# Kernel tuning notes

Hardware: AMD Instinct MI355X
Metric: run time of the kernel (lower is better)

## Reference

```python
import jax, jax.numpy as jnp
import numpy as np

DELAY = 4
SKIP = 2
NF = 8
HS = 256
EPS = 1e-5


def setup_inputs() -> dict:
    key = jax.random.key(0)
    ks = jax.random.split(key, 11)
    B, NP, NO, T = 16, 512, 512, 2048
    predictor = jax.random.normal(ks[0], (B, NP, T), dtype=jnp.float32)
    to_order = jax.random.normal(ks[1], (B, NO, T), dtype=jnp.float32)
    trilinear = jax.random.normal(ks[2], (NF, NO, NP), dtype=jnp.float32) / np.float32(np.sqrt(NP * NO))
    w_o = jax.random.normal(ks[3], (HS, NO), dtype=jnp.float32) / np.float32(np.sqrt(NO))
    b_o = jax.random.normal(ks[4], (HS,), dtype=jnp.float32) * 0.01
    w_p = jax.random.normal(ks[5], (HS, NP), dtype=jnp.float32) / np.float32(np.sqrt(NP))
    b_p = jax.random.normal(ks[6], (HS,), dtype=jnp.float32) * 0.01
    bn_gamma = jnp.ones((HS,), dtype=jnp.float32)
    bn_beta = jnp.zeros((HS,), dtype=jnp.float32)
    w_out = jax.random.normal(ks[7], (NF, HS), dtype=jnp.float32) / np.float32(np.sqrt(HS))
    b_out = jax.random.normal(ks[8], (NF,), dtype=jnp.float32) * 0.01
    return {"predictor": predictor, "to_order": to_order, "trilinear": trilinear,
            "w_o": w_o, "b_o": b_o, "w_p": w_p, "b_p": b_p,
            "bn_gamma": bn_gamma, "bn_beta": bn_beta, "w_out": w_out, "b_out": b_out}


def reference(predictor, to_order, trilinear, w_o, b_o, w_p, b_p, bn_gamma, bn_beta, w_out, b_out):
    B, NP, T = predictor.shape
    NO = to_order.shape[1]
    tot_latency = DELAY + SKIP * (NF - 1)
    T_r = T - tot_latency
    pred = predictor[:, :, :T_r]          # (B, np, Tr)
    too = to_order[:, :, DELAY:]          # (B, no, T - delay)
    # predictor_product[b,k,t,m] = sum_p pred[b,p,t] * trilinear[k,m,p]
    pp = jnp.einsum('bpt,kmp->bktm', pred, trilinear)           # (B, nf, Tr, no)
    win = jnp.stack([too[:, :, j * SKIP: j * SKIP + T_r] for j in range(NF)], axis=1)  # (B, nf, no, Tr)
    inner = jnp.einsum('bjmt,bktm->bjkt', win, pp)              # (B, nf, nf, Tr)
    # conv1d (kernel 1) heads
    o_proj = jnp.einsum('hm,bmt->bht', w_o, too) + b_o[None, :, None]    # (B, hs, T - delay)
    p_proj = jnp.einsum('hp,bpt->bht', w_p, pred) + b_p[None, :, None]   # (B, hs, Tr)
    o_win = jnp.stack([o_proj[:, :, j * SKIP: j * SKIP + T_r] for j in range(NF)], axis=1)  # (B, nf, hs, Tr)
    h = jax.nn.relu(o_win + p_proj[:, None])                    # (B, nf, hs, Tr)
    # BatchNorm1d (training-mode batch stats) over (B*nf, hs, Tr): stats over axes (0,1,3)
    mean = h.mean(axis=(0, 1, 3), keepdims=True)
    var = h.var(axis=(0, 1, 3), keepdims=True)
    h = (h - mean) * jax.lax.rsqrt(var + EPS) * bn_gamma[None, None, :, None] + bn_beta[None, None, :, None]
    head = jnp.einsum('kh,bjht->bjkt', w_out, h) + b_out[None, None, :, None]
    inner = inner + head
    log_probs = jax.nn.log_softmax(inner, axis=2)               # (B, nf, nf, Tr)
    correct = jnp.einsum('bjjt->bjt', log_probs)                # diagonal j == k
    return correct.mean(axis=2).mean(axis=0)                    # (nf,)
```

## Files before the change

### kernel.cpp

```cpp
#include <hip/hip_runtime.h>
#include <math.h>

constexpr int B_  = 16;
constexpr int NP_ = 512;
constexpr int NO_ = 512;
constexpr int T_  = 2048;
constexpr int NF_ = 8;
constexpr int HS_ = 256;
constexpr int TR_ = 2030;
constexpr int TO_ = 2044;
constexpr int OPLD_ = 2048;
constexpr float EPS_ = 1e-5f;

typedef short bf16x8 __attribute__((ext_vector_type(8)));
typedef float f32x16 __attribute__((ext_vector_type(16)));

__device__ __forceinline__ unsigned short f2bf(float f) {
  union { float f; unsigned int u; } v; v.f = f;
  unsigned int r = v.u + 0x7fffu + ((v.u >> 16) & 1u);
  return (unsigned short)(r >> 16);
}
__device__ __forceinline__ float bf2f(unsigned short u) {
  union { unsigned int u; float f; } v; v.u = ((unsigned int)u) << 16;
  return v.f;
}

typedef const __attribute__((address_space(1))) unsigned int* gas_u32;
typedef __attribute__((address_space(3))) unsigned int* las_u32;
__device__ __forceinline__ void gl16(const void* g, void* l) {
  __builtin_amdgcn_global_load_lds((gas_u32)g, (las_u32)l, 16, 0, 0);
}


__global__ __launch_bounds__(256) void transpose_cvt(
    const float* __restrict__ in, unsigned short* __restrict__ outb) {
  __shared__ float tile[64][65];
  const int c0 = blockIdx.x * 64;
  const int r0 = blockIdx.y * 64;
  const int b  = blockIdx.z;
  const float* ib = in + (size_t)b * 512 * 2048;
  unsigned short* ob = outb + (size_t)b * 2048 * 512;
  for (int i = threadIdx.x; i < 64 * 16; i += 256) {
    const int r = i >> 4, c4 = (i & 15) * 4;
    float4 v = *(const float4*)(ib + (size_t)(r0 + r) * 2048 + c0 + c4);
    tile[r][c4 + 0] = v.x; tile[r][c4 + 1] = v.y;
    tile[r][c4 + 2] = v.z; tile[r][c4 + 3] = v.w;
  }
  __syncthreads();
  for (int i = threadIdx.x; i < 64 * 8; i += 256) {
    const int c = i >> 3, r8 = (i & 7) * 8;
    unsigned int pk[4];
    #pragma unroll
    for (int e = 0; e < 4; ++e)
      pk[e] = (unsigned int)f2bf(tile[r8 + 2 * e][c]) |
              ((unsigned int)f2bf(tile[r8 + 2 * e + 1][c]) << 16);
    *(uint4*)(ob + (size_t)(c0 + c) * 512 + r0 + r8) = *(uint4*)pk;
  }
}

__global__ __launch_bounds__(256) void cvt_bf16(
    const float* __restrict__ in, unsigned short* __restrict__ out, int n) {
  const int i = (blockIdx.x * 256 + threadIdx.x) * 4;
  if (i < n) {
    float4 v = *(const float4*)(in + i);
    ushort4 o; o.x = f2bf(v.x); o.y = f2bf(v.y); o.z = f2bf(v.z); o.w = f2bf(v.w);
    *(ushort4*)(out + i) = o;
  }
}

__global__ __launch_bounds__(256, 2) void proj_mfma(
    const unsigned short* __restrict__ Wbf,
    const unsigned short* __restrict__ Xt,
    const float* __restrict__ bias,
    unsigned short* __restrict__ out,
    int Tlen, int toff) {
  __shared__ char smem[65536];
  char* const Ab[2] = { smem, smem + 16384 };
  char* const Bb[2] = { smem + 32768, smem + 49152 };
  const int tid = threadIdx.x;
  const int l = tid & 63, wv = tid >> 6;
  const int h = l >> 5, tl = l & 31;
  const int mq = wv >> 1, tq = wv & 1;
  const int t0 = blockIdx.x * 128;
  const int m0 = blockIdx.y * 128;
  const int b  = blockIdx.z;
  const unsigned short* Xb = Xt + (size_t)b * T_ * 512;

  int aSrc[4], bSrc[4], ldsO[4];
  #pragma unroll
  for (int i = 0; i < 4; ++i) {
    const int q = (wv << 8) + (i << 6) + l;
    const int r = q >> 3, c8s = (q & 7) ^ (r & 7);
    aSrc[i] = (m0 + r) * 512 + (c8s << 3);
    const int row = min(t0 + toff + r, T_ - 1);
    bSrc[i] = row * 512 + (c8s << 3);
    ldsO[i] = ((wv << 8) + (i << 6)) << 4;
  }

  f32x16 acc[2][2];
  #pragma unroll
  for (int i = 0; i < 2; ++i)
    #pragma unroll
    for (int jj = 0; jj < 2; ++jj)
      #pragma unroll
      for (int e = 0; e < 16; ++e) acc[i][jj][e] = 0.f;

  #pragma unroll
  for (int i = 0; i < 4; ++i) gl16(Wbf + aSrc[i], Ab[0] + ldsO[i]);
  #pragma unroll
  for (int i = 0; i < 4; ++i) gl16(Xb + bSrc[i], Bb[0] + ldsO[i]);
  asm volatile("s_waitcnt vmcnt(0)" ::: "memory");
  __builtin_amdgcn_s_barrier();

  #pragma unroll
  for (int ps = 0; ps < 8; ++ps) {
    const int cb = ps & 1;
    if (ps < 7) {
      const int p0 = (ps + 1) << 6;
      #pragma unroll
      for (int i = 0; i < 4; ++i) gl16(Wbf + p0 + aSrc[i], Ab[cb ^ 1] + ldsO[i]);
      #pragma unroll
      for (int i = 0; i < 4; ++i) gl16(Xb + p0 + bSrc[i], Bb[cb ^ 1] + ldsO[i]);
    }
    const unsigned short* As = (const unsigned short*)Ab[cb];
    const unsigned short* Bs = (const unsigned short*)Bb[cb];
    #pragma unroll
    for (int s = 0; s < 4; ++s) {
      const int k8 = 2 * s + h;
      bf16x8 af[2], bfr[2];
      #pragma unroll
      for (int mt = 0; mt < 2; ++mt) {
        const int rm = 64 * mq + 32 * mt + tl;
        af[mt] = *(const bf16x8*)(As + rm * 64 + ((k8 ^ (rm & 7)) << 3));
      }
      #pragma unroll
      for (int nt = 0; nt < 2; ++nt) {
        const int rt = 64 * tq + 32 * nt + tl;
        bfr[nt] = *(const bf16x8*)(Bs + rt * 64 + ((k8 ^ (rt & 7)) << 3));
      }
      #pragma unroll
      for (int mt = 0; mt < 2; ++mt)
        #pragma unroll
        for (int nt = 0; nt < 2; ++nt)
          acc[mt][nt] = __builtin_amdgcn_mfma_f32_32x32x16_bf16(
              af[mt], bfr[nt], acc[mt][nt], 0, 0, 0);
    }
    asm volatile("s_waitcnt vmcnt(0)" ::: "memory");
    __builtin_amdgcn_s_barrier();
  }
  #pragma unroll
  for (int mt = 0; mt < 2; ++mt)
    #pragma unroll
    for (int nt = 0; nt < 2; ++nt)
      #pragma unroll
      for (int r = 0; r < 16; ++r) {
        const int hs = m0 + 64 * mq + 32 * mt + (r & 3) + 8 * (r >> 2) + 4 * h;
        const int t  = t0 + 64 * tq + 32 * nt + tl;
        if (t < Tlen)
          out[((size_t)b * HS_ + hs) * OPLD_ + t] = f2bf(acc[mt][nt][r] + bias[hs]);
      }
}

__global__ __launch_bounds__(256, 2) void inner_mfma(
    const unsigned short* __restrict__ pred_t,
    const unsigned short* __restrict__ too_t,
    const unsigned short* __restrict__ tri_bf,
    float* __restrict__ inner) {
  __shared__ char smem[77824];
  char* const Pb[2] = { smem, smem + 16384 };
  char* const Tb[2] = { smem + 32768, smem + 49152 };
  char* const TOOM  = smem + 65536;
  char* const TAIL  = smem + 32768;
  const int tid = threadIdx.x;
  const int l = tid & 63, wv = tid >> 6;
  const int h = l >> 5, tl = l & 31;
  const int t0 = blockIdx.x * 128;
  const int kf0 = blockIdx.y * 2;
  const int b  = blockIdx.z;
  const unsigned short* predB = pred_t + (size_t)b * T_ * NP_;
  const unsigned short* tooB  = too_t  + (size_t)b * T_ * NO_;
  const unsigned short* triK  = tri_bf + (size_t)kf0 * NO_ * NP_;

  int pSrc[4], pLds[4];
  #pragma unroll
  for (int i = 0; i < 4; ++i) {
    const int q = (wv << 8) + (i << 6) + l;
    const int r = q >> 3, c8s = (q & 7) ^ (r & 7);
    pSrc[i] = (t0 + r) * NP_ + (c8s << 3);
    pLds[i] = ((wv << 8) + (i << 6)) << 4;
  }
  int tSrc[4], tLds[4];
  #pragma unroll
  for (int i = 0; i < 4; ++i) {
    const int q = (wv << 8) + (i << 6) + l;
    const int f = q >> 9, qq = q & 511;
    const int r = qq >> 3, c8s = (qq & 7) ^ (r & 7);
    tSrc[i] = f * (NO_ * NP_) + r * NP_ + (c8s << 3);
    tLds[i] = ((wv << 8) + (i << 6)) << 4;
  }
  int oSrc[3], oLds[3];
  #pragma unroll
  for (int i = 0; i < 3; ++i) {
    const int q = wv * 192 + (i << 6) + l;
    const int r = q >> 3, c8s = (q & 7) ^ (r & 7);
    oSrc[i] = (t0 + r) * NO_ + (c8s << 3);
    oLds[i] = (wv * 192 + (i << 6)) << 4;
  }
  int aSrcT[4], aLdsT[4];
  {
    const int ws = (wv >= 2) ? (wv - 2) : 0;
    #pragma unroll
    for (int i = 0; i < 4; ++i) {
      const int q = (ws << 8) + (i << 6) + l;
      const int r = 96 + (q >> 3), c8s = (q & 7) ^ (r & 7);
      aSrcT[i] = min(t0 + r, T_ - 1) * NO_ + (c8s << 3);
      aLdsT[i] = ((ws << 8) + (i << 6)) << 4;
    }
  }

  f32x16 Sacc[2][2];
  #pragma unroll
  for (int f = 0; f < 2; ++f)
    #pragma unroll
    for (int ct = 0; ct < 2; ++ct)
      #pragma unroll
      for (int e = 0; e < 16; ++e) Sacc[f][ct][e] = 0.f;

  for (int mc = 0; mc < 8; ++mc) {
    const int m0 = mc << 6;
    const int mOff = m0 * NP_;
    __builtin_amdgcn_s_barrier();
    #pragma unroll
    for (int i = 0; i < 3; ++i) gl16(tooB + m0 + oSrc[i], TOOM + oLds[i]);
    #pragma unroll
    for (int i = 0; i < 4; ++i) gl16(triK + mOff + tSrc[i], Tb[0] + tLds[i]);
    #pragma unroll
    for (int i = 0; i < 4; ++i) gl16(predB + pSrc[i], Pb[0] + pLds[i]);
    asm volatile("s_waitcnt vmcnt(0)" ::: "memory");
    __builtin_amdgcn_s_barrier();

    f32x16 Qacc[2][2];
    #pragma unroll
    for (int f = 0; f < 2; ++f)
      #pragma unroll
      for (int mt = 0; mt < 2; ++mt)
        #pragma unroll
        for (int e = 0; e < 16; ++e) Qacc[f][mt][e] = 0.f;

    #pragma unroll
    for (int ps = 0; ps < 8; ++ps) {
      const int cb = ps & 1;
      if (ps < 7) {
        const int p1 = (ps + 1) << 6;
        #pragma unroll
        for (int i = 0; i < 4; ++i)
          gl16(triK + mOff + p1 + tSrc[i], Tb[cb ^ 1] + tLds[i]);
        #pragma unroll
        for (int i = 0; i < 4; ++i)
          gl16(predB + p1 + pSrc[i], Pb[cb ^ 1] + pLds[i]);
      }
      const unsigned short* predS = (const unsigned short*)Pb[cb];
      const unsigned short* triS  = (const unsigned short*)Tb[cb];
      #pragma unroll
      for (int s = 0; s < 4; ++s) {
        const int k8 = 2 * s + h;
        const int rb = (wv << 5) + tl;
        const bf16x8 bp = *(const bf16x8*)(predS + rb * 64 + ((k8 ^ (rb & 7)) << 3));
        #pragma unroll
        for (int mt = 0; mt < 2; ++mt) {
          const int rm = (mt << 5) + tl;
          const int co = rm * 64 + ((k8 ^ (rm & 7)) << 3);
          const bf16x8 a0 = *(const bf16x8*)(triS + co);
          const bf16x8 a1 = *(const bf16x8*)(triS + 2048 + co);
          Qacc[0][mt] = __builtin_amdgcn_mfma_f32_32x32x16_bf16(a0, bp, Qacc[0][mt], 0, 0, 0);
          Qacc[1][mt] = __builtin_amdgcn_mfma_f32_32x32x16_bf16(a1, bp, Qacc[1][mt], 0, 0, 0);
        }
      }
      if (ps == 7 && wv >= 2) {
        #pragma unroll
        for (int i = 0; i < 4; ++i)
          gl16(tooB + m0 + aSrcT[i], TAIL + aLdsT[i]);
      }
      asm volatile("s_waitcnt vmcnt(0)" ::: "memory");
      __builtin_amdgcn_s_barrier();
    }
    #pragma unroll
    for (int f = 0; f < 2; ++f) {
      unsigned short* QSw = (unsigned short*)(Pb[f] + (wv << 12));
      #pragma unroll
      for (int mt = 0; mt < 2; ++mt)
        #pragma unroll
        for (int rp = 0; rp < 8; ++rp) {
          const int r = rp << 1;
          const int m = (mt << 5) + (r & 3) + ((r >> 2) << 3) + (h << 2);
          const int c8 = m >> 3, ml = m & 7;
          const int rX = (tl & 24) | ((tl ^ c8) & 7);
          const unsigned int pk = (unsigned int)f2bf(Qacc[f][mt][r]) |
                                  ((unsigned int)f2bf(Qacc[f][mt][r + 1]) << 16);
          *(unsigned int*)(QSw + (((c8 << 5) + rX) << 3) + ml) = pk;
        }
    }
    #pragma unroll
    for (int s = 0; s < 4; ++s) {
      const int k8 = 2 * s + h;
      bf16x8 atoo[2];
      #pragma unroll
      for (int ct = 0; ct < 2; ++ct) {
        const int rbase = (wv + ct) << 5;
        const int rr = rbase + tl;
        const unsigned short* tb = (rbase < 96)
            ? (const unsigned short*)TOOM + (size_t)rr * 64
            : (const unsigned short*)TAIL + (size_t)(rr - 96) * 64;
        atoo[ct] = *(const bf16x8*)(tb + ((k8 ^ (rr & 7)) << 3));
      }
      const int rqX = (tl & 24) | ((tl ^ k8) & 7);
      #pragma unroll
      for (int f = 0; f < 2; ++f) {
        const bf16x8 bq = *(const bf16x8*)((const unsigned short*)(Pb[f] + (wv << 12)) +
                                           (((k8 << 5) + rqX) << 3));
        #pragma unroll
        for (int ct = 0; ct < 2; ++ct)
          Sacc[f][ct] = __builtin_amdgcn_mfma_f32_32x32x16_bf16(atoo[ct], bq, Sacc[f][ct], 0, 0, 0);
      }
    }
  }
  __syncthreads();
  const int tglob = t0 + (wv << 5) + tl;
  float* SW = (float*)smem + (wv << 11);
  #pragma unroll
  for (int f = 0; f < 2; ++f) {
    #pragma unroll
    for (int ct = 0; ct < 2; ++ct)
      #pragma unroll
      for (int r = 0; r < 16; ++r) {
        const int cc = (ct << 5) + (r & 3) + ((r >> 2) << 3) + (h << 2);
        SW[(cc << 5) + tl] = Sacc[f][ct][r];
      }
    if (tglob < TR_) {
      #pragma unroll
      for (int jj = 0; jj < 4; ++jj) {
        const int j = (jj << 1) + h;
        const float v = SW[((tl + 4 + 2 * j) << 5) + tl];
        inner[(((size_t)b * NF_ + j) * NF_ + (kf0 + f)) * TR_ + tglob] = v;
      }
    }
  }
}

__global__ __launch_bounds__(256) void bn_stats(
    const unsigned short* __restrict__ op, const unsigned short* __restrict__ pp,
    float* __restrict__ partials) {
  const int hh = blockIdx.x, b = blockIdx.y;
  const unsigned short* oprow = op + ((size_t)b * HS_ + hh) * OPLD_;
  const unsigned short* pprow = pp + ((size_t)b * HS_ + hh) * OPLD_;
  float s = 0.f, s2 = 0.f;
  for (int t = threadIdx.x; t < TR_; t += 256) {
    const float pv = bf2f(pprow[t]);
    #pragma unroll
    for (int j = 0; j < NF_; ++j) {
      float r = bf2f(oprow[t + 2 * j]) + pv;
      r = fmaxf(r, 0.f);
      s += r; s2 += r * r;
    }
  }
  __shared__ float red[256], red2[256];
  red[threadIdx.x] = s; red2[threadIdx.x] = s2;
  __syncthreads();
  for (int st = 128; st > 0; st >>= 1) {
    if (threadIdx.x < st) {
      red[threadIdx.x]  += red[threadIdx.x + st];
      red2[threadIdx.x] += red2[threadIdx.x + st];
    }
    __syncthreads();
  }
  if (threadIdx.x == 0) {
    partials[b * HS_ + hh]            = red[0];
    partials[B_ * HS_ + b * HS_ + hh] = red2[0];
  }
}

__global__ __launch_bounds__(256) void bn_finalize(
    const float* __restrict__ partials, const float* __restrict__ gamma,
    const float* __restrict__ beta, const float* __restrict__ w_out,
    const float* __restrict__ b_out, float* __restrict__ w_eff,
    float* __restrict__ cvec) {
  const int hh = threadIdx.x;
  float s = 0.f, s2 = 0.f;
  for (int b = 0; b < B_; ++b) {
    s  += partials[b * HS_ + hh];
    s2 += partials[B_ * HS_ + b * HS_ + hh];
  }
  const float cnt  = (float)B_ * NF_ * TR_;
  const float mean = s / cnt;
  const float var  = s2 / cnt - mean * mean;
  const float scale = gamma[hh] * rsqrtf(var + EPS_);
  const float shift = beta[hh] - mean * scale;
  #pragma unroll
  for (int k = 0; k < NF_; ++k) w_eff[k * HS_ + hh] = w_out[k * HS_ + hh] * scale;
  __shared__ float red[256];
  for (int k = 0; k < NF_; ++k) {
    red[hh] = w_out[k * HS_ + hh] * shift;
    __syncthreads();
    for (int st = 128; st > 0; st >>= 1) {
      if (hh < st) red[hh] += red[hh + st];
      __syncthreads();
    }
    if (hh == 0) cvec[k] = b_out[k] + red[0];
    __syncthreads();
  }
}

__global__ __launch_bounds__(256) void head_final(
    const unsigned short* __restrict__ op, const unsigned short* __restrict__ pp,
    const float* __restrict__ w_eff, const float* __restrict__ cvec,
    const float* __restrict__ inner, float* __restrict__ part3) {
  __shared__ float opS[288 * 20];
  __shared__ float ppS[256 * 20];
  __shared__ float weS[8][256];
  __shared__ float red[4][5];
  const int tid = threadIdx.x;
  const int t0 = blockIdx.x * 256;
  const int b  = blockIdx.y;
  const int jh = blockIdx.z;
  for (int i = tid; i < 8 * 256; i += 256) weS[i >> 8][i & 255] = w_eff[i];
  float acc[4][8] = {};
  const unsigned short* opb = op + (size_t)b * HS_ * OPLD_;
  const unsigned short* ppb = pp + (size_t)b * HS_ * OPLD_;
  for (int hc = 0; hc < 16; ++hc) {
    const int h0 = hc << 4;
    __syncthreads();
    for (int idx = tid; idx < 576; idx += 256) {
      const int r = idx / 36, cc = (idx - r * 36) << 3;
      const int g = min(t0 + cc, OPLD_ - 8);
      uint4 v = *(const uint4*)(opb + (size_t)(h0 + r) * OPLD_ + g);
      #pragma unroll
      for (int e = 0; e < 4; ++e) {
        const unsigned int u = (&v.x)[e];
        opS[(cc + 2 * e) * 20 + r]     = bf2f((unsigned short)(u & 0xffffu));
        opS[(cc + 2 * e + 1) * 20 + r] = bf2f((unsigned short)(u >> 16));
      }
    }
    for (int idx = tid; idx < 512; idx += 256) {
      const int r = idx >> 5, cc = (idx & 31) << 3;
      uint4 v = *(const uint4*)(ppb + (size_t)(h0 + r) * OPLD_ + t0 + cc);
      #pragma unroll
      for (int e = 0; e < 4; ++e) {
        const unsigned int u = (&v.x)[e];
        ppS[(cc + 2 * e) * 20 + r]     = bf2f((unsigned short)(u & 0xffffu));
        ppS[(cc + 2 * e + 1) * 20 + r] = bf2f((unsigned short)(u >> 16));
      }
    }
    __syncthreads();
    float pv[16];
    #pragma unroll
    for (int i = 0; i < 4; ++i) {
      float4 q = *(const float4*)(ppS + tid * 20 + 4 * i);
      pv[4 * i + 0] = q.x; pv[4 * i + 1] = q.y;
      pv[4 * i + 2] = q.z; pv[4 * i + 3] = q.w;
    }
    #pragma unroll
    for (int jj = 0; jj < 4; ++jj) {
      const int col = tid + 2 * ((jh << 2) + jj);
      #pragma unroll
      for (int i = 0; i < 4; ++i) {
        float4 ov = *(const float4*)(opS + col * 20 + 4 * i);
        #pragma unroll
        for (int e = 0; e < 4; ++e) {
          const float r = fmaxf((&ov.x)[e] + pv[4 * i + e], 0.f);
          #pragma unroll
          for (int k = 0; k < 8; ++k) acc[jj][k] += weS[k][h0 + 4 * i + e] * r;
        }
      }
    }
  }
  const int t = t0 + tid;
  float sj[4];
  #pragma unroll
  for (int jj = 0; jj < 4; ++jj) {
    if (t < TR_) {
      const int j = (jh << 2) + jj;
      float v[8]; float mx = -1e30f;
      #pragma unroll
      for (int k = 0; k < 8; ++k) {
        v[k] = acc[jj][k] + cvec[k] +
               inner[(((size_t)b * NF_ + j) * NF_ + k) * TR_ + t];
        mx = fmaxf(mx, v[k]);
      }
      float se = 0.f;
      #pragma unroll
      for (int k = 0; k < 8; ++k) se += expf(v[k] - mx);
      sj[jj] = v[j] - mx - logf(se);
    } else sj[jj] = 0.f;
  }
  #pragma unroll
  for (int jj = 0; jj < 4; ++jj)
    #pragma unroll
    for (int off = 32; off > 0; off >>= 1) sj[jj] += __shfl_down(sj[jj], off);
  if ((tid & 63) == 0) {
    const int wv = tid >> 6;
    #pragma unroll
    for (int jj = 0; jj < 4; ++jj) red[jj][wv] = sj[jj];
  }
  __syncthreads();
  if (tid < 4) {
    const float s = red[tid][0] + red[tid][1] + red[tid][2] + red[tid][3];
    const int j = (jh << 2) + tid;
    part3[(j * B_ + b) * 8 + blockIdx.x] = s;
  }
}

__global__ void final_out(const float* __restrict__ part3, float* __restrict__ out) {
  const int j = threadIdx.x;
  if (j < NF_) {
    float s = 0.f;
    for (int i = 0; i < B_ * 8; ++i) s += part3[j * B_ * 8 + i];
    out[j] = s / ((float)B_ * (float)TR_);
  }
}

extern "C" void kernel_launch(void* const* d_in, const int* in_sizes, int n_in,
                              void* d_out, int out_size, void* d_ws, size_t ws_size,
                              hipStream_t stream) {
  const float* predictor = (const float*)d_in[0];
  const float* to_order  = (const float*)d_in[1];
  const float* trilinear = (const float*)d_in[2];
  const float* w_o   = (const float*)d_in[3];
  const float* b_o   = (const float*)d_in[4];
  const float* w_p   = (const float*)d_in[5];
  const float* b_p   = (const float*)d_in[6];
  const float* bn_g  = (const float*)d_in[7];
  const float* bn_b  = (const float*)d_in[8];
  const float* w_out = (const float*)d_in[9];
  const float* b_out = (const float*)d_in[10];
  float* out = (float*)d_out;

  char* w = (char*)d_ws;
  unsigned short* pred_t = (unsigned short*)w; w += (size_t)B_ * T_ * NP_ * 2;
  unsigned short* too_t  = (unsigned short*)w; w += (size_t)B_ * T_ * NO_ * 2;
  unsigned short* tri_bf = (unsigned short*)w; w += (size_t)NF_ * NO_ * NP_ * 2;
  unsigned short* wo_bf  = (unsigned short*)w; w += (size_t)HS_ * NO_ * 2;
  unsigned short* wp_bf  = (unsigned short*)w; w += (size_t)HS_ * NP_ * 2;
  unsigned short* o_proj = (unsigned short*)w; w += (size_t)B_ * HS_ * OPLD_ * 2;
  unsigned short* p_proj = (unsigned short*)w; w += (size_t)B_ * HS_ * OPLD_ * 2;
  float* inner    = (float*)w; w += (size_t)B_ * NF_ * NF_ * TR_ * 4;
  float* partials = (float*)w; w += (size_t)2 * B_ * HS_ * 4;
  float* w_eff    = (float*)w; w += (size_t)NF_ * HS_ * 4;
  float* cvec     = (float*)w; w += 256;
  float* part3    = (float*)w; w += (size_t)NF_ * B_ * 8 * 4;

  transpose_cvt<<<dim3(32, 8, 16), 256, 0, stream>>>(predictor, pred_t);
  transpose_cvt<<<dim3(32, 8, 16), 256, 0, stream>>>(to_order, too_t);
  cvt_bf16<<<2048, 256, 0, stream>>>(trilinear, tri_bf, NF_ * NO_ * NP_);
  cvt_bf16<<<128, 256, 0, stream>>>(w_o, wo_bf, HS_ * NO_);
  cvt_bf16<<<128, 256, 0, stream>>>(w_p, wp_bf, HS_ * NP_);

  proj_mfma<<<dim3(16, 2, 16), 256, 0, stream>>>(wo_bf, too_t, b_o, o_proj, TO_, 4);
  proj_mfma<<<dim3(16, 2, 16), 256, 0, stream>>>(wp_bf, pred_t, b_p, p_proj, TR_, 0);

  inner_mfma<<<dim3(16, 4, 16), 256, 0, stream>>>(pred_t, too_t, tri_bf, inner);

  bn_stats<<<dim3(HS_, B_), 256, 0, stream>>>(o_proj, p_proj, partials);
  bn_finalize<<<1, 256, 0, stream>>>(partials, bn_g, bn_b, w_out, b_out, w_eff, cvec);
  head_final<<<dim3(8, B_, 2), 256, 0, stream>>>(o_proj, p_proj, w_eff, cvec, inner, part3);
  final_out<<<1, 64, 0, stream>>>(part3, out);
}
```

Before: 338.2 us.

## Triple-buffer predictor tiles and re-split waves across features and time in inner_mfma

inner_mfma now loads predictor tiles into a three-slot ring two stages ahead, with partial vmcnt waits, instead of double buffering with a full drain every step. Each wave now computes a 2x2 MFMA tile over one feature and half the time rows, so a/b fragments are reused across two MFMAs each. The to_order operand for the second GEMM is read straight from global memory rather than staged through LDS. s_setprio is raised around the MFMA loop. This trades LDS staging of to_order for uncoalesced direct global loads and raises shared memory use to 80 KB per block, which may lower occupancy.

After: 371.3 us. 1.1x slower.

```diff
diff --git a/kernel.cpp b/kernel.cpp
--- a/kernel.cpp
+++ b/kernel.cpp
@@ -75,8 +75,6 @@
     unsigned short* __restrict__ out,
     int Tlen, int toff) {
   __shared__ char smem[65536];
-  char* const Ab[2] = { smem, smem + 16384 };
-  char* const Bb[2] = { smem + 32768, smem + 49152 };
   const int tid = threadIdx.x;
   const int l = tid & 63, wv = tid >> 6;
   const int h = l >> 5, tl = l & 31;
@@ -106,9 +104,9 @@
       for (int e = 0; e < 16; ++e) acc[i][jj][e] = 0.f;
 
   #pragma unroll
-  for (int i = 0; i < 4; ++i) gl16(Wbf + aSrc[i], Ab[0] + ldsO[i]);
-  #pragma unroll
-  for (int i = 0; i < 4; ++i) gl16(Xb + bSrc[i], Bb[0] + ldsO[i]);
+  for (int i = 0; i < 4; ++i) gl16(Wbf + aSrc[i], smem + ldsO[i]);
+  #pragma unroll
+  for (int i = 0; i < 4; ++i) gl16(Xb + bSrc[i], smem + 32768 + ldsO[i]);
   asm volatile("s_waitcnt vmcnt(0)" ::: "memory");
   __builtin_amdgcn_s_barrier();
 
@@ -118,12 +116,14 @@
     if (ps < 7) {
       const int p0 = (ps + 1) << 6;
       #pragma unroll
-      for (int i = 0; i < 4; ++i) gl16(Wbf + p0 + aSrc[i], Ab[cb ^ 1] + ldsO[i]);
-      #pragma unroll
-      for (int i = 0; i < 4; ++i) gl16(Xb + p0 + bSrc[i], Bb[cb ^ 1] + ldsO[i]);
-    }
-    const unsigned short* As = (const unsigned short*)Ab[cb];
-    const unsigned short* Bs = (const unsigned short*)Bb[cb];
+      for (int i = 0; i < 4; ++i)
+        gl16(Wbf + p0 + aSrc[i], smem + (cb ^ 1) * 16384 + ldsO[i]);
+      #pragma unroll
+      for (int i = 0; i < 4; ++i)
+        gl16(Xb + p0 + bSrc[i], smem + 32768 + (cb ^ 1) * 16384 + ldsO[i]);
+    }
+    const unsigned short* As = (const unsigned short*)(smem + cb * 16384);
+    const unsigned short* Bs = (const unsigned short*)(smem + 32768 + cb * 16384);
     #pragma unroll
     for (int s = 0; s < 4; ++s) {
       const int k8 = 2 * s + h;
@@ -166,14 +166,11 @@
     const unsigned short* __restrict__ too_t,
     const unsigned short* __restrict__ tri_bf,
     float* __restrict__ inner) {
-  __shared__ char smem[77824];
-  char* const Pb[2] = { smem, smem + 16384 };
-  char* const Tb[2] = { smem + 32768, smem + 49152 };
-  char* const TOOM  = smem + 65536;
-  char* const TAIL  = smem + 32768;
+  __shared__ char smem[81920];
   const int tid = threadIdx.x;
   const int l = tid & 63, wv = tid >> 6;
   const int h = l >> 5, tl = l & 31;
+  const int fk = wv & 1, th = wv >> 1;
   const int t0 = blockIdx.x * 128;
   const int kf0 = blockIdx.y * 2;
   const int b  = blockIdx.z;
@@ -198,25 +195,6 @@
     tSrc[i] = f * (NO_ * NP_) + r * NP_ + (c8s << 3);
     tLds[i] = ((wv << 8) + (i << 6)) << 4;
   }
-  int oSrc[3], oLds[3];
-  #pragma unroll
-  for (int i = 0; i < 3; ++i) {
-    const int q = wv * 192 + (i << 6) + l;
-    const int r = q >> 3, c8s = (q & 7) ^ (r & 7);
-    oSrc[i] = (t0 + r) * NO_ + (c8s << 3);
-    oLds[i] = (wv * 192 + (i << 6)) << 4;
-  }
-  int aSrcT[4], aLdsT[4];
-  {
-    const int ws = (wv >= 2) ? (wv - 2) : 0;
-    #pragma unroll
-    for (int i = 0; i < 4; ++i) {
-      const int q = (ws << 8) + (i << 6) + l;
-      const int r = 96 + (q >> 3), c8s = (q & 7) ^ (r & 7);
-      aSrcT[i] = min(t0 + r, T_ - 1) * NO_ + (c8s << 3);
-      aLdsT[i] = ((ws << 8) + (i << 6)) << 4;
-    }
-  }
 
   f32x16 Sacc[2][2];
   #pragma unroll
@@ -231,62 +209,72 @@
     const int mOff = m0 * NP_;
     __builtin_amdgcn_s_barrier();
     #pragma unroll
-    for (int i = 0; i < 3; ++i) gl16(tooB + m0 + oSrc[i], TOOM + oLds[i]);
-    #pragma unroll
-    for (int i = 0; i < 4; ++i) gl16(triK + mOff + tSrc[i], Tb[0] + tLds[i]);
-    #pragma unroll
-    for (int i = 0; i < 4; ++i) gl16(predB + pSrc[i], Pb[0] + pLds[i]);
-    asm volatile("s_waitcnt vmcnt(0)" ::: "memory");
-    __builtin_amdgcn_s_barrier();
+    for (int i = 0; i < 4; ++i) gl16(triK + mOff + tSrc[i], smem + 49152 + tLds[i]);
+    #pragma unroll
+    for (int i = 0; i < 4; ++i) gl16(predB + pSrc[i], smem + pLds[i]);
+    #pragma unroll
+    for (int i = 0; i < 4; ++i) gl16(predB + 64 + pSrc[i], smem + 16384 + pLds[i]);
 
     f32x16 Qacc[2][2];
     #pragma unroll
-    for (int f = 0; f < 2; ++f)
-      #pragma unroll
-      for (int mt = 0; mt < 2; ++mt)
-        #pragma unroll
-        for (int e = 0; e < 16; ++e) Qacc[f][mt][e] = 0.f;
+    for (int mt = 0; mt < 2; ++mt)
+      #pragma unroll
+      for (int nt = 0; nt < 2; ++nt)
+        #pragma unroll
+        for (int e = 0; e < 16; ++e) Qacc[mt][nt][e] = 0.f;
 
     #pragma unroll
     for (int ps = 0; ps < 8; ++ps) {
       const int cb = ps & 1;
+      if (ps < 7) asm volatile("s_waitcnt vmcnt(4)" ::: "memory");
+      else        asm volatile("s_waitcnt vmcnt(0)" ::: "memory");
+      __builtin_amdgcn_s_barrier();
       if (ps < 7) {
         const int p1 = (ps + 1) << 6;
         #pragma unroll
         for (int i = 0; i < 4; ++i)
-          gl16(triK + mOff + p1 + tSrc[i], Tb[cb ^ 1] + tLds[i]);
+          gl16(triK + mOff + p1 + tSrc[i],
+               smem + 49152 + (cb ^ 1) * 16384 + tLds[i]);
+      }
+      if (ps < 6) {
+        const int p2 = (ps + 2) << 6;
+        char* const pb2 = smem + ((ps + 2) % 3) * 16384;
         #pragma unroll
         for (int i = 0; i < 4; ++i)
-          gl16(predB + p1 + pSrc[i], Pb[cb ^ 1] + pLds[i]);
-      }
-      const unsigned short* predS = (const unsigned short*)Pb[cb];
-      const unsigned short* triS  = (const unsigned short*)Tb[cb];
+          gl16(predB + p2 + pSrc[i], pb2 + pLds[i]);
+      }
+      const unsigned short* predS = (const unsigned short*)(smem + (ps % 3) * 16384);
+      const unsigned short* triS  = (const unsigned short*)(smem + 49152 + cb * 16384);
+      __builtin_amdgcn_s_setprio(1);
       #pragma unroll
       for (int s = 0; s < 4; ++s) {
         const int k8 = 2 * s + h;
-        const int rb = (wv << 5) + tl;
-        const bf16x8 bp = *(const bf16x8*)(predS + rb * 64 + ((k8 ^ (rb & 7)) << 3));
+        bf16x8 a[2], bp[2];
         #pragma unroll
         for (int mt = 0; mt < 2; ++mt) {
           const int rm = (mt << 5) + tl;
-          const int co = rm * 64 + ((k8 ^ (rm & 7)) << 3);
-          const bf16x8 a0 = *(const bf16x8*)(triS + co);
-          const bf16x8 a1 = *(const bf16x8*)(triS + 2048 + co);
-          Qacc[0][mt] = __builtin_amdgcn_mfma_f32_32x32x16_bf16(a0, bp, Qacc[0][mt], 0, 0, 0);
-          Qacc[1][mt] = __builtin_amdgcn_mfma_f32_32x32x16_bf16(a1, bp, Qacc[1][mt], 0, 0, 0);
+          a[mt] = *(const bf16x8*)(triS + (fk << 12) + rm * 64 +
+                                   ((k8 ^ (rm & 7)) << 3));
         }
-      }
-      if (ps == 7 && wv >= 2) {
-        #pragma unroll
-        for (int i = 0; i < 4; ++i)
-          gl16(tooB + m0 + aSrcT[i], TAIL + aLdsT[i]);
-      }
-      asm volatile("s_waitcnt vmcnt(0)" ::: "memory");
-      __builtin_amdgcn_s_barrier();
-    }
-    #pragma unroll
-    for (int f = 0; f < 2; ++f) {
-      unsigned short* QSw = (unsigned short*)(Pb[f] + (wv << 12));
+        #pragma unroll
+        for (int nt = 0; nt < 2; ++nt) {
+          const int rb = (th << 6) + (nt << 5) + tl;
+          bp[nt] = *(const bf16x8*)(predS + rb * 64 + ((k8 ^ (rb & 7)) << 3));
+        }
+        #pragma unroll
+        for (int mt = 0; mt < 2; ++mt)
+          #pragma unroll
+          for (int nt = 0; nt < 2; ++nt)
+            Qacc[mt][nt] = __builtin_amdgcn_mfma_f32_32x32x16_bf16(
+                a[mt], bp[nt], Qacc[mt][nt], 0, 0, 0);
+      }
+      __builtin_amdgcn_s_setprio(0);
+    }
+    __builtin_amdgcn_s_barrier();
+    #pragma unroll
+    for (int nt = 0; nt < 2; ++nt) {
+      unsigned short* QSw =
+          (unsigned short*)(smem + fk * 16384 + (((th << 1) + nt) << 12));
       #pragma unroll
       for (int mt = 0; mt < 2; ++mt)
         #pragma unroll
@@ -295,32 +283,33 @@
           const int m = (mt << 5) + (r & 3) + ((r >> 2) << 3) + (h << 2);
           const int c8 = m >> 3, ml = m & 7;
           const int rX = (tl & 24) | ((tl ^ c8) & 7);
-          const unsigned int pk = (unsigned int)f2bf(Qacc[f][mt][r]) |
-                                  ((unsigned int)f2bf(Qacc[f][mt][r + 1]) << 16);
+          const unsigned int pk = (unsigned int)f2bf(Qacc[mt][nt][r]) |
+                                  ((unsigned int)f2bf(Qacc[mt][nt][r + 1]) << 16);
           *(unsigned int*)(QSw + (((c8 << 5) + rX) << 3) + ml) = pk;
         }
     }
+    asm volatile("s_waitcnt lgkmcnt(0)" ::: "memory");
+    __builtin_amdgcn_s_barrier();
     #pragma unroll
     for (int s = 0; s < 4; ++s) {
       const int k8 = 2 * s + h;
       bf16x8 atoo[2];
       #pragma unroll
       for (int ct = 0; ct < 2; ++ct) {
-        const int rbase = (wv + ct) << 5;
-        const int rr = rbase + tl;
-        const unsigned short* tb = (rbase < 96)
-            ? (const unsigned short*)TOOM + (size_t)rr * 64
-            : (const unsigned short*)TAIL + (size_t)(rr - 96) * 64;
-        atoo[ct] = *(const bf16x8*)(tb + ((k8 ^ (rr & 7)) << 3));
+        const int rr = ((wv + ct) << 5) + tl;
+        const int trow = min(t0 + rr, T_ - 1);
+        atoo[ct] = *(const bf16x8*)(tooB + (size_t)trow * NO_ + m0 + (k8 << 3));
       }
       const int rqX = (tl & 24) | ((tl ^ k8) & 7);
       #pragma unroll
       for (int f = 0; f < 2; ++f) {
-        const bf16x8 bq = *(const bf16x8*)((const unsigned short*)(Pb[f] + (wv << 12)) +
-                                           (((k8 << 5) + rqX) << 3));
+        const bf16x8 bq = *(const bf16x8*)(
+            (const unsigned short*)(smem + f * 16384 + (wv << 12)) +
+            (((k8 << 5) + rqX) << 3));
         #pragma unroll
         for (int ct = 0; ct < 2; ++ct)
-          Sacc[f][ct] = __builtin_amdgcn_mfma_f32_32x32x16_bf16(atoo[ct], bq, Sacc[f][ct], 0, 0, 0);
+          Sacc[f][ct] = __builtin_amdgcn_mfma_f32_32x32x16_bf16(
+              atoo[ct], bq, Sacc[f][ct], 0, 0, 0);
       }
     }
   }
```
